# Kernel optimization log

Hardware: AMD Instinct MI355X
Metric: run time of the kernel (lower is better)

Reference implementation:

```python
import jax, jax.numpy as jnp
import numpy as np

IN_DIM = 1024
OUT_DIM = 1024
HIDDEN = 1024
T = 16384
R_MIN, R_MAX, MAX_PHASE = 0.9, 0.999, 6.28


@jax.vmap
def binary_operator_diag(q_i, q_j):
    A_i, b_i = q_i
    A_j, b_j = q_j
    return (A_j * A_i, A_j * b_i + b_j)


def setup_inputs() -> dict:
    key = jax.random.key(0)
    ks = jax.random.split(key, 8)
    inputs = jax.random.normal(ks[0], (T, IN_DIM), dtype=jnp.float32)
    # nu_log / theta_log per original initializers
    u1 = jax.random.uniform(ks[1], (HIDDEN,), dtype=jnp.float32)
    nu_log = jnp.log(-0.5 * jnp.log(u1 * (R_MAX ** 2 - R_MIN ** 2) + R_MIN ** 2))
    u2 = jax.random.uniform(ks[2], (HIDDEN,), dtype=jnp.float32)
    theta_log = jnp.log(MAX_PHASE * u2)
    diag_lambda = jnp.exp(-jnp.exp(nu_log) + 1j * jnp.exp(theta_log))
    gamma_log = jnp.log(jnp.sqrt(1 - jnp.abs(diag_lambda) ** 2))
    B_re = jax.random.normal(ks[3], (IN_DIM, HIDDEN), dtype=jnp.float32) / jnp.sqrt(2.0 * IN_DIM)
    B_im = jax.random.normal(ks[4], (IN_DIM, HIDDEN), dtype=jnp.float32) / jnp.sqrt(2.0 * IN_DIM)
    C_re = jax.random.normal(ks[5], (OUT_DIM, HIDDEN), dtype=jnp.float32) / jnp.sqrt(1.0 * HIDDEN)
    C_im = jax.random.normal(ks[6], (OUT_DIM, HIDDEN), dtype=jnp.float32) / jnp.sqrt(1.0 * HIDDEN)
    D = jax.random.normal(ks[7], (OUT_DIM, IN_DIM), dtype=jnp.float32)
    return {"inputs": inputs, "nu_log": nu_log, "theta_log": theta_log,
            "gamma_log": gamma_log, "B_re": B_re, "B_im": B_im,
            "C_re": C_re, "C_im": C_im, "D": D}


def reference(inputs, nu_log, theta_log, gamma_log, B_re, B_im, C_re, C_im, D):
    # diagonal complex transition eigenvalues, shape (H,)
    diag_lambda = jnp.exp(-jnp.exp(nu_log) + 1j * jnp.exp(theta_log))
    # NOTE: original code expands gamma on axis=-1 -> (H, 1); broadcasts against
    # B_norm (in_dim, H) because in_dim == hidden_dim. Reproduced faithfully.
    B_norm = (B_re + 1j * B_im) * jnp.exp(gamma_log)[:, None]
    C = C_re + 1j * C_im
    T_len = inputs.shape[-2]
    Lambda_elements = jnp.repeat(diag_lambda[None, :], T_len, axis=0)  # (T, H)
    Bu_elements = jnp.einsum('ih,ti->th', B_norm, inputs)              # (T, H) complex
    _, hidden_states = jax.lax.associative_scan(
        binary_operator_diag, (Lambda_elements, Bu_elements))
    outputs = jnp.real(jnp.einsum('th,oh->to', hidden_states, C))      # (T, out)
    outputs = outputs + jnp.einsum('ti,io->to', inputs, D)             # D used as 'io'
    return outputs
```

## Files before the change

kernel.cpp:

```cpp
#include <hip/hip_runtime.h>
#include <hip/hip_bf16.h>
#include <stdint.h>

#define T_LEN   16384
#define HID     1024
#define KDIM    1024
#define CHUNK   64
#define NCHUNK  256

typedef __bf16 bf16x8 __attribute__((ext_vector_type(8)));
typedef float  f32x4  __attribute__((ext_vector_type(4)));

__device__ inline ushort f2bf(float f) {
  union { float f; uint32_t u; } v; v.f = f;
  uint32_t r = v.u + 0x7FFF + ((v.u >> 16) & 1);
  return (ushort)(r >> 16);
}
__device__ inline float bf2f(ushort u) {
  union { uint32_t u; float f; } v; v.u = ((uint32_t)u) << 16;
  return v.f;
}

__device__ inline void gload16(const void* g, void* l) {
  __builtin_amdgcn_global_load_lds(
      (const __attribute__((address_space(1))) void*)g,
      (__attribute__((address_space(3))) void*)l, 16, 0, 0);
}

__global__ __launch_bounds__(256) void prep_kernel(
    const float* __restrict__ nu_log, const float* __restrict__ theta_log,
    const float* __restrict__ gamma_log,
    float* __restrict__ lam_re, float* __restrict__ lam_im, float* __restrict__ eg) {
  int h = blockIdx.x * 256 + threadIdx.x;
  if (h < HID) {
    float mag = expf(-expf(nu_log[h]));
    float th  = expf(theta_log[h]);
    lam_re[h] = mag * cosf(th);
    lam_im[h] = mag * sinf(th);
    eg[h]     = expf(gamma_log[h]);
  }
}

__global__ __launch_bounds__(256) void convX(
    const float* __restrict__ src, ushort* __restrict__ dst) {
  size_t i = ((size_t)blockIdx.x * 256 + threadIdx.x) * 4;
  float4 v = *(const float4*)(src + i);
  ushort4 o;
  o.x = f2bf(v.x); o.y = f2bf(v.y); o.z = f2bf(v.z); o.w = f2bf(v.w);
  *(ushort4*)(dst + i) = o;
}

__global__ __launch_bounds__(256) void weight_prep(
    const float* __restrict__ Bre, const float* __restrict__ Bim,
    const float* __restrict__ Cre, const float* __restrict__ Cim,
    const float* __restrict__ D,   const float* __restrict__ eg,
    ushort* __restrict__ BreT, ushort* __restrict__ BimT,
    ushort* __restrict__ CreB, ushort* __restrict__ CimB,
    ushort* __restrict__ DT) {
  __shared__ float tile[32][33];
  int z = blockIdx.z;
  if (z == 2 || z == 3) {
    const float* src = (z == 2) ? Cre : Cim;
    ushort* dst = (z == 2) ? CreB : CimB;
    float s = (z == 2) ? 1.0f : -1.0f;
    size_t base = ((size_t)blockIdx.y * 32 + (threadIdx.x >> 3)) * 1024 +
                  blockIdx.x * 32 + (threadIdx.x & 7) * 4;
    float4 v = *(const float4*)(src + base);
    ushort4 o;
    o.x = f2bf(v.x * s); o.y = f2bf(v.y * s);
    o.z = f2bf(v.z * s); o.w = f2bf(v.w * s);
    *(ushort4*)(dst + base) = o;
    return;
  }
  const float* src = (z == 0) ? Bre : (z == 1) ? Bim : D;
  ushort* dst = (z == 0) ? BreT : (z == 1) ? BimT : DT;
  bool scaled = (z < 2);
  int bx = blockIdx.x * 32;
  int by = blockIdx.y * 32;
  int tx = threadIdx.x & 31, ty = threadIdx.x >> 5;
#pragma unroll
  for (int r = 0; r < 32; r += 8)
    tile[ty + r][tx] = src[(size_t)(by + ty + r) * 1024 + bx + tx];
  __syncthreads();
  float sc = scaled ? eg[by + tx] : 1.0f;
#pragma unroll
  for (int r = 0; r < 32; r += 8)
    dst[(size_t)(bx + ty + r) * 1024 + by + tx] = f2bf(tile[tx][ty + r] * sc);
}


#define BAR()   __builtin_amdgcn_s_barrier()
#define FEN()   asm volatile("" ::: "memory")
#define VM4()   asm volatile("s_waitcnt vmcnt(4)" ::: "memory")
#define VM0()   asm volatile("s_waitcnt vmcnt(0)" ::: "memory")
#define PBAR()  do { FEN(); BAR(); FEN(); } while (0)

#define STAGE_HALF(G, LDA, R0, K0, LT, HALF)                         \
  do {                                                               \
    _Pragma("unroll")                                                \
    for (int is_ = 0; is_ < 2; ++is_) {                              \
      int seg_ = w * 2 + is_;                                        \
      int gr_ = (R0) + (HALF) * 128 + seg_ * 8 + (l >> 3);           \
      int gc_ = (K0) + (((l & 7) ^ (l >> 3)) << 3);                  \
      gload16((G) + (size_t)gr_ * (LDA) + gc_,                       \
              (LT) + (HALF) * 8192 + seg_ * 512);                    \
    }                                                                \
  } while (0)

#define DS_A(QM, BUF)                                                \
  do {                                                               \
    _Pragma("unroll")                                                \
    for (int m_ = 0; m_ < 4; ++m_) {                                 \
      int r_ = (wr * 128 + ((QM) * 4 + m_) * 16 + lo) * 64;          \
      a[m_][0] = *(const bf16x8*)((BUF) + r_ + c0us);                \
      a[m_][1] = *(const bf16x8*)((BUF) + r_ + c1us);                \
    }                                                                \
  } while (0)

#define DS_B(QN, BUF, REG)                                           \
  do {                                                               \
    _Pragma("unroll")                                                \
    for (int n_ = 0; n_ < 2; ++n_) {                                 \
      int r_ = (wc * 64 + ((QN) * 2 + n_) * 16 + lo) * 64;           \
      REG[n_][0] = *(const bf16x8*)((BUF) + r_ + c0us);              \
      REG[n_][1] = *(const bf16x8*)((BUF) + r_ + c1us);              \
    }                                                                \
  } while (0)

#define MFMA_Q(QM, QN, REG)                                          \
  do {                                                               \
    __builtin_amdgcn_s_setprio(1);                                   \
    _Pragma("unroll")                                                \
    for (int m_ = 0; m_ < 4; ++m_)                                   \
      _Pragma("unroll")                                              \
      for (int n_ = 0; n_ < 2; ++n_) {                               \
        f32x4* ac_ = &acc[(QM) * 4 + m_][(QN) * 2 + n_];             \
        *ac_ = __builtin_amdgcn_mfma_f32_16x16x32_bf16(              \
            a[m_][0], REG[n_][0], *ac_, 0, 0, 0);                    \
        *ac_ = __builtin_amdgcn_mfma_f32_16x16x32_bf16(              \
            a[m_][1], REG[n_][1], *ac_, 0, 0, 0);                    \
      }                                                              \
    __builtin_amdgcn_s_setprio(0);                                   \
  } while (0)

template<int NSEG>
__device__ __forceinline__ void gemm256_1bar(
    const ushort* Ap0, int ld0, const ushort* Bp0,
    const ushort* Ap1, int ld1, const ushort* Bp1,
    const ushort* Ap2, int ld2, const ushort* Bp2,
    ushort* lds, int row0, int col0,
    int w, int l, int wr, int wc, int lo, int c0us, int c1us,
    f32x4 (&acc)[8][4]) {
  ushort* A0 = lds;
  ushort* A1 = lds + 16384;
  ushort* B0 = lds + 32768;
  ushort* B1 = lds + 49152;
  bf16x8 a[4][2], bq0[2][2], bq1[2][2];
  const int NT = NSEG * 16;

  auto stageA = [&](int t, ushort* buf) {
    const ushort* A; int lda;
    if constexpr (NSEG == 1) { A = Ap0; lda = ld0; }
    else {
      if (t < 16)      { A = Ap0; lda = ld0; }
      else if (t < 32) { A = Ap1; lda = ld1; }
      else             { A = Ap2; lda = ld2; }
    }
    const int kk = (t & 15) * 64;
    STAGE_HALF(A, lda, row0, kk, buf, 0);
    STAGE_HALF(A, lda, row0, kk, buf, 1);
  };
  auto stageB = [&](int t, ushort* buf) {
    const ushort* B;
    if constexpr (NSEG == 1) { B = Bp0; }
    else {
      if (t < 16)      B = Bp0;
      else if (t < 32) B = Bp1;
      else             B = Bp2;
    }
    const int kk = (t & 15) * 64;
    STAGE_HALF(B, 1024, col0, kk, buf, 0);
    STAGE_HALF(B, 1024, col0, kk, buf, 1);
  };

  stageA(0, A0); stageB(0, B0); stageB(1, B1);
  VM4(); PBAR();

#pragma unroll 1
  for (int j = 0; j < NT / 2; ++j) {
    const int t1 = 2 * j + 1, t2 = 2 * j + 2, t3 = 2 * j + 3;
    const bool st = (t2 < NT);
    DS_A(0, A0); DS_B(0, B0, bq0);
    stageA(t1, A1);
    PBAR(); MFMA_Q(0, 0, bq0);
    DS_B(1, B0, bq1);
    PBAR(); MFMA_Q(0, 1, bq1);
    DS_A(1, A0);
    PBAR(); MFMA_Q(1, 0, bq0);
    if (st) { stageB(t2, B0); VM4(); } else { VM0(); }
    PBAR(); MFMA_Q(1, 1, bq1);
    DS_A(0, A1); DS_B(0, B1, bq0);
    if (st) stageA(t2, A0);
    PBAR(); MFMA_Q(0, 0, bq0);
    DS_B(1, B1, bq1);
    PBAR(); MFMA_Q(0, 1, bq1);
    DS_A(1, A1);
    PBAR(); MFMA_Q(1, 0, bq0);
    if (st) { stageB(t3, B1); VM4(); }
    PBAR(); MFMA_Q(1, 1, bq1);
  }
}

__global__ __launch_bounds__(512, 2) void gemm_bu(
    const ushort* __restrict__ A, const ushort* __restrict__ B,
    ushort* __restrict__ O) {
  __shared__ __align__(16) ushort lds[65536];
  const int tid = threadIdx.x;
  const int w = tid >> 6, l = tid & 63;
  const int wr = w >> 2, wc = w & 3;
  const int lo = l & 15, q = l >> 4;
  const int xorv = (lo & 7) << 4;
  const int c0us = ((q * 16) ^ xorv) >> 1;
  const int c1us = ((64 + q * 16) ^ xorv) >> 1;
  const int id = blockIdx.x;
  const int xcd = id & 7, slot = id >> 3;
  const int row0 = (xcd * 8 + (slot >> 3)) * 256;
  const int col0 = (slot & 7) * 256;
  f32x4 acc[8][4];
#pragma unroll
  for (int m = 0; m < 8; ++m)
#pragma unroll
    for (int n = 0; n < 4; ++n) acc[m][n] = (f32x4){0.f, 0.f, 0.f, 0.f};
  gemm256_1bar<1>(A, 1024, B, A, 1024, B, A, 1024, B,
                  lds, row0, col0, w, l, wr, wc, lo, c0us, c1us, acc);
  const int rowb = row0 + wr * 128, colb = col0 + wc * 64;
#pragma unroll
  for (int m = 0; m < 8; ++m)
#pragma unroll
    for (int n = 0; n < 4; ++n) {
      int col = colb + n * 16 + lo;
#pragma unroll
      for (int r = 0; r < 4; ++r)
        O[(size_t)(rowb + m * 16 + q * 4 + r) * 2048 + col] = f2bf(acc[m][n][r]);
    }
}

__global__ __launch_bounds__(512, 2) void gemm3(
    const ushort* __restrict__ Hall,
    const ushort* __restrict__ CreB, const ushort* __restrict__ CimB,
    const ushort* __restrict__ X,    const ushort* __restrict__ DT,
    float* __restrict__ O) {
  __shared__ __align__(16) ushort lds[65536];
  const int tid = threadIdx.x;
  const int w = tid >> 6, l = tid & 63;
  const int wr = w >> 2, wc = w & 3;
  const int lo = l & 15, q = l >> 4;
  const int xorv = (lo & 7) << 4;
  const int c0us = ((q * 16) ^ xorv) >> 1;
  const int c1us = ((64 + q * 16) ^ xorv) >> 1;
  const int id = blockIdx.x;
  const int xcd = id & 7, slot = id >> 3;
  const int row0 = (xcd * 8 + (slot >> 2)) * 256;
  const int col0 = (slot & 3) * 256;
  f32x4 acc[8][4];
#pragma unroll
  for (int m = 0; m < 8; ++m)
#pragma unroll
    for (int n = 0; n < 4; ++n) acc[m][n] = (f32x4){0.f, 0.f, 0.f, 0.f};
  gemm256_1bar<3>(Hall, 2048, CreB,
                  Hall + 1024, 2048, CimB,
                  X, 1024, DT,
                  lds, row0, col0, w, l, wr, wc, lo, c0us, c1us, acc);
  const int rowb = row0 + wr * 128, colb = col0 + wc * 64;
#pragma unroll
  for (int m = 0; m < 8; ++m)
#pragma unroll
    for (int n = 0; n < 4; ++n) {
      int col = colb + n * 16 + lo;
#pragma unroll
      for (int r = 0; r < 4; ++r)
        O[(size_t)(rowb + m * 16 + q * 4 + r) * HID + col] = acc[m][n][r];
    }
}

__global__ __launch_bounds__(256) void scan_sums(
    const ushort* __restrict__ Bu,
    const float* __restrict__ lam_re, const float* __restrict__ lam_im,
    float* __restrict__ Sre, float* __restrict__ Sim) {
  int h0 = (blockIdx.y * 256 + threadIdx.x) * 2;
  int c = blockIdx.x;
  float lr0 = lam_re[h0], li0 = lam_im[h0];
  float lr1 = lam_re[h0 + 1], li1 = lam_im[h0 + 1];
  float hr0 = 0.f, hi0 = 0.f, hr1 = 0.f, hi1 = 0.f;
  const uint* P = (const uint*)Bu;
  size_t baseR = (size_t)c * CHUNK * 1024 + (h0 >> 1);
  size_t baseI = baseR + 512;
#pragma unroll 8
  for (int t = 0; t < CHUNK; ++t) {
    uint re = P[baseR + (size_t)t * 1024];
    uint im = P[baseI + (size_t)t * 1024];
    float br0 = bf2f((ushort)re), br1 = bf2f((ushort)(re >> 16));
    float bi0 = bf2f((ushort)im), bi1 = bf2f((ushort)(im >> 16));
    float nr0 = fmaf(lr0, hr0, fmaf(-li0, hi0, br0));
    float ni0 = fmaf(lr0, hi0, fmaf(li0, hr0, bi0));
    float nr1 = fmaf(lr1, hr1, fmaf(-li1, hi1, br1));
    float ni1 = fmaf(lr1, hi1, fmaf(li1, hr1, bi1));
    hr0 = nr0; hi0 = ni0; hr1 = nr1; hi1 = ni1;
  }
  Sre[(size_t)c * HID + h0] = hr0;  Sre[(size_t)c * HID + h0 + 1] = hr1;
  Sim[(size_t)c * HID + h0] = hi0;  Sim[(size_t)c * HID + h0 + 1] = hi1;
}

__global__ __launch_bounds__(256) void scan_carry(
    const float* __restrict__ Sre, const float* __restrict__ Sim,
    const float* __restrict__ lam_re, const float* __restrict__ lam_im,
    float* __restrict__ Pre, float* __restrict__ Pim) {
  int h = blockIdx.x * 256 + threadIdx.x;
  float lr = lam_re[h], li = lam_im[h];
  float pr = lr, pi = li;
#pragma unroll
  for (int s = 0; s < 6; ++s) {
    float nr = pr * pr - pi * pi;
    float ni = 2.f * pr * pi;
    pr = nr; pi = ni;
  }
  float cr = 0.f, ci = 0.f;
  for (int c = 0; c < NCHUNK; ++c) {
    Pre[(size_t)c * HID + h] = cr;
    Pim[(size_t)c * HID + h] = ci;
    float sr = Sre[(size_t)c * HID + h];
    float si = Sim[(size_t)c * HID + h];
    float nr = fmaf(pr, cr, fmaf(-pi, ci, sr));
    float ni = fmaf(pr, ci, fmaf(pi, cr, si));
    cr = nr; ci = ni;
  }
}

__global__ __launch_bounds__(256) void scan_emit(
    const ushort* __restrict__ Bu,
    const float* __restrict__ lam_re, const float* __restrict__ lam_im,
    const float* __restrict__ Pre, const float* __restrict__ Pim,
    ushort* __restrict__ Hall) {
  int h0 = (blockIdx.y * 256 + threadIdx.x) * 2;
  int c = blockIdx.x;
  float lr0 = lam_re[h0], li0 = lam_im[h0];
  float lr1 = lam_re[h0 + 1], li1 = lam_im[h0 + 1];
  float hr0 = Pre[(size_t)c * HID + h0], hi0 = Pim[(size_t)c * HID + h0];
  float hr1 = Pre[(size_t)c * HID + h0 + 1], hi1 = Pim[(size_t)c * HID + h0 + 1];
  const uint* P = (const uint*)Bu;
  uint* Q = (uint*)Hall;
  size_t baseR = (size_t)c * CHUNK * 1024 + (h0 >> 1);
  size_t baseI = baseR + 512;
#pragma unroll 8
  for (int t = 0; t < CHUNK; ++t) {
    uint re = P[baseR + (size_t)t * 1024];
    uint im = P[baseI + (size_t)t * 1024];
    float br0 = bf2f((ushort)re), br1 = bf2f((ushort)(re >> 16));
    float bi0 = bf2f((ushort)im), bi1 = bf2f((ushort)(im >> 16));
    float nr0 = fmaf(lr0, hr0, fmaf(-li0, hi0, br0));
    float ni0 = fmaf(lr0, hi0, fmaf(li0, hr0, bi0));
    float nr1 = fmaf(lr1, hr1, fmaf(-li1, hi1, br1));
    float ni1 = fmaf(lr1, hi1, fmaf(li1, hr1, bi1));
    hr0 = nr0; hi0 = ni0; hr1 = nr1; hi1 = ni1;
    Q[baseR + (size_t)t * 1024] = (uint)f2bf(hr0) | ((uint)f2bf(hr1) << 16);
    Q[baseI + (size_t)t * 1024] = (uint)f2bf(hi0) | ((uint)f2bf(hi1) << 16);
  }
}

extern "C" void kernel_launch(void* const* d_in, const int* in_sizes, int n_in,
                              void* d_out, int out_size, void* d_ws, size_t ws_size,
                              hipStream_t stream) {
  const float* inputs    = (const float*)d_in[0];
  const float* nu_log    = (const float*)d_in[1];
  const float* theta_log = (const float*)d_in[2];
  const float* gamma_log = (const float*)d_in[3];
  const float* B_re      = (const float*)d_in[4];
  const float* B_im      = (const float*)d_in[5];
  const float* C_re      = (const float*)d_in[6];
  const float* C_im      = (const float*)d_in[7];
  const float* D         = (const float*)d_in[8];
  float* out = (float*)d_out;

  char* ws = (char*)d_ws;
  constexpr size_t TH = (size_t)T_LEN * HID;
  constexpr size_t W  = (size_t)1024 * 1024;
  constexpr size_t CH = (size_t)NCHUNK * HID;

  ushort* Xbf  = (ushort*)(ws);
  ushort* Bu   = (ushort*)(ws + TH * 2);
  ushort* Hall = (ushort*)(ws + TH * 6);
  char*   p    = ws + TH * 10;
  ushort* Ball = (ushort*)(p);             p += 2 * W * 2;
  ushort* CreB = (ushort*)(p);             p += W * 2;
  ushort* CimB = (ushort*)(p);             p += W * 2;
  ushort* DT   = (ushort*)(p);             p += W * 2;
  float*  Sre  = (float*)(p);              p += CH * 4;
  float*  Sim  = (float*)(p);              p += CH * 4;
  float*  Pre  = (float*)(p);              p += CH * 4;
  float*  Pim  = (float*)(p);              p += CH * 4;
  float*  lamR = (float*)(p);              p += 4096;
  float*  lamI = (float*)(p);              p += 4096;
  float*  eg   = (float*)(p);              p += 4096;
  ushort* BreT = Ball;
  ushort* BimT = Ball + W;

  prep_kernel<<<dim3(HID / 256), 256, 0, stream>>>(nu_log, theta_log, gamma_log,
                                                   lamR, lamI, eg);
  convX<<<dim3((unsigned)(TH / 4 / 256)), 256, 0, stream>>>(inputs, Xbf);
  weight_prep<<<dim3(32, 32, 5), 256, 0, stream>>>(B_re, B_im, C_re, C_im, D, eg,
                                                   BreT, BimT, CreB, CimB, DT);

  gemm_bu<<<dim3(512), 512, 0, stream>>>(Xbf, Ball, Bu);

  scan_sums<<<dim3(NCHUNK, HID / 512), 256, 0, stream>>>(Bu, lamR, lamI, Sre, Sim);
  scan_carry<<<dim3(HID / 256), 256, 0, stream>>>(Sre, Sim, lamR, lamI, Pre, Pim);
  scan_emit<<<dim3(NCHUNK, HID / 512), 256, 0, stream>>>(Bu, lamR, lamI, Pre, Pim,
                                                         Hall);

  gemm3<<<dim3(256), 512, 0, stream>>>(Hall, CreB, CimB, Xbf, DT, out);
}
```

Before: 340.9 us.

## Merge prep kernels and fold scan carry pass into emit kernel

Fuses the three preprocessing kernels (lambda computation, input bf16 conversion, weight transpose/scale) into one launch with a z-indexed dispatch, computing exp(gamma) inline. Removes the serial scan_carry kernel; each scan_emit block instead recomputes its chunk prefix by walking all earlier chunk sums, and scan kernels now process 4 hidden units per thread with wider loads. This trades two launches and a single-threaded serial carry pass for redundant O(c) carry work per chunk (later chunks do up to 255 steps).

Measured after the change: 378.3 us. 1.11x slower.

```diff
diff --git a/kernel.cpp b/kernel.cpp
--- a/kernel.cpp
+++ b/kernel.cpp
@@ -27,44 +27,46 @@
       (__attribute__((address_space(3))) void*)l, 16, 0, 0);
 }
 
-__global__ __launch_bounds__(256) void prep_kernel(
+__global__ __launch_bounds__(256) void prep_all(
+    const float* __restrict__ inputs,
     const float* __restrict__ nu_log, const float* __restrict__ theta_log,
     const float* __restrict__ gamma_log,
-    float* __restrict__ lam_re, float* __restrict__ lam_im, float* __restrict__ eg) {
-  int h = blockIdx.x * 256 + threadIdx.x;
-  if (h < HID) {
-    float mag = expf(-expf(nu_log[h]));
-    float th  = expf(theta_log[h]);
-    lam_re[h] = mag * cosf(th);
-    lam_im[h] = mag * sinf(th);
-    eg[h]     = expf(gamma_log[h]);
-  }
-}
-
-__global__ __launch_bounds__(256) void convX(
-    const float* __restrict__ src, ushort* __restrict__ dst) {
-  size_t i = ((size_t)blockIdx.x * 256 + threadIdx.x) * 4;
-  float4 v = *(const float4*)(src + i);
-  ushort4 o;
-  o.x = f2bf(v.x); o.y = f2bf(v.y); o.z = f2bf(v.z); o.w = f2bf(v.w);
-  *(ushort4*)(dst + i) = o;
-}
-
-__global__ __launch_bounds__(256) void weight_prep(
     const float* __restrict__ Bre, const float* __restrict__ Bim,
     const float* __restrict__ Cre, const float* __restrict__ Cim,
-    const float* __restrict__ D,   const float* __restrict__ eg,
+    const float* __restrict__ D,
+    ushort* __restrict__ Xbf,
     ushort* __restrict__ BreT, ushort* __restrict__ BimT,
     ushort* __restrict__ CreB, ushort* __restrict__ CimB,
-    ushort* __restrict__ DT) {
+    ushort* __restrict__ DT,
+    float* __restrict__ lam_re, float* __restrict__ lam_im) {
   __shared__ float tile[32][33];
-  int z = blockIdx.z;
+  const int z = blockIdx.z;
+  const int tid = threadIdx.x;
+  if (z >= 6) {
+    size_t b = (size_t)(z - 6) * 1024 + blockIdx.y * 32 + blockIdx.x;
+    size_t i = (b * 256 + tid) * 4;
+    float4 v = *(const float4*)(inputs + i);
+    ushort4 o;
+    o.x = f2bf(v.x); o.y = f2bf(v.y); o.z = f2bf(v.z); o.w = f2bf(v.w);
+    *(ushort4*)(Xbf + i) = o;
+    return;
+  }
+  if (z == 5) {
+    if (blockIdx.y == 0 && blockIdx.x < 4) {
+      int h = blockIdx.x * 256 + tid;
+      float mag = expf(-expf(nu_log[h]));
+      float th  = expf(theta_log[h]);
+      lam_re[h] = mag * cosf(th);
+      lam_im[h] = mag * sinf(th);
+    }
+    return;
+  }
   if (z == 2 || z == 3) {
     const float* src = (z == 2) ? Cre : Cim;
     ushort* dst = (z == 2) ? CreB : CimB;
     float s = (z == 2) ? 1.0f : -1.0f;
-    size_t base = ((size_t)blockIdx.y * 32 + (threadIdx.x >> 3)) * 1024 +
-                  blockIdx.x * 32 + (threadIdx.x & 7) * 4;
+    size_t base = ((size_t)blockIdx.y * 32 + (tid >> 3)) * 1024 +
+                  blockIdx.x * 32 + (tid & 7) * 4;
     float4 v = *(const float4*)(src + base);
     ushort4 o;
     o.x = f2bf(v.x * s); o.y = f2bf(v.y * s);
@@ -77,17 +79,16 @@
   bool scaled = (z < 2);
   int bx = blockIdx.x * 32;
   int by = blockIdx.y * 32;
-  int tx = threadIdx.x & 31, ty = threadIdx.x >> 5;
+  int tx = tid & 31, ty = tid >> 5;
 #pragma unroll
   for (int r = 0; r < 32; r += 8)
     tile[ty + r][tx] = src[(size_t)(by + ty + r) * 1024 + bx + tx];
   __syncthreads();
-  float sc = scaled ? eg[by + tx] : 1.0f;
+  float sc = scaled ? expf(gamma_log[by + tx]) : 1.0f;
 #pragma unroll
   for (int r = 0; r < 32; r += 8)
     dst[(size_t)(bx + ty + r) * 1024 + by + tx] = f2bf(tile[tx][ty + r] * sc);
 }
-
 
 #define BAR()   __builtin_amdgcn_s_barrier()
 #define FEN()   asm volatile("" ::: "memory")
@@ -287,83 +288,92 @@
     const ushort* __restrict__ Bu,
     const float* __restrict__ lam_re, const float* __restrict__ lam_im,
     float* __restrict__ Sre, float* __restrict__ Sim) {
-  int h0 = (blockIdx.y * 256 + threadIdx.x) * 2;
-  int c = blockIdx.x;
-  float lr0 = lam_re[h0], li0 = lam_im[h0];
-  float lr1 = lam_re[h0 + 1], li1 = lam_im[h0 + 1];
-  float hr0 = 0.f, hi0 = 0.f, hr1 = 0.f, hi1 = 0.f;
-  const uint* P = (const uint*)Bu;
-  size_t baseR = (size_t)c * CHUNK * 1024 + (h0 >> 1);
-  size_t baseI = baseR + 512;
+  const int c = blockIdx.x, tid = threadIdx.x;
+  const int h0 = tid * 4;
+  float lr[4], li[4], hr[4], hi[4];
+#pragma unroll
+  for (int j = 0; j < 4; ++j) {
+    lr[j] = lam_re[h0 + j]; li[j] = lam_im[h0 + j];
+    hr[j] = 0.f; hi[j] = 0.f;
+  }
+  const uint2* R = (const uint2*)Bu;
+  size_t rb = (size_t)c * CHUNK * 512;
 #pragma unroll 8
   for (int t = 0; t < CHUNK; ++t) {
-    uint re = P[baseR + (size_t)t * 1024];
-    uint im = P[baseI + (size_t)t * 1024];
-    float br0 = bf2f((ushort)re), br1 = bf2f((ushort)(re >> 16));
-    float bi0 = bf2f((ushort)im), bi1 = bf2f((ushort)(im >> 16));
-    float nr0 = fmaf(lr0, hr0, fmaf(-li0, hi0, br0));
-    float ni0 = fmaf(lr0, hi0, fmaf(li0, hr0, bi0));
-    float nr1 = fmaf(lr1, hr1, fmaf(-li1, hi1, br1));
-    float ni1 = fmaf(lr1, hi1, fmaf(li1, hr1, bi1));
-    hr0 = nr0; hi0 = ni0; hr1 = nr1; hi1 = ni1;
-  }
-  Sre[(size_t)c * HID + h0] = hr0;  Sre[(size_t)c * HID + h0 + 1] = hr1;
-  Sim[(size_t)c * HID + h0] = hi0;  Sim[(size_t)c * HID + h0 + 1] = hi1;
-}
-
-__global__ __launch_bounds__(256) void scan_carry(
-    const float* __restrict__ Sre, const float* __restrict__ Sim,
-    const float* __restrict__ lam_re, const float* __restrict__ lam_im,
-    float* __restrict__ Pre, float* __restrict__ Pim) {
-  int h = blockIdx.x * 256 + threadIdx.x;
-  float lr = lam_re[h], li = lam_im[h];
-  float pr = lr, pi = li;
-#pragma unroll
-  for (int s = 0; s < 6; ++s) {
-    float nr = pr * pr - pi * pi;
-    float ni = 2.f * pr * pi;
-    pr = nr; pi = ni;
-  }
-  float cr = 0.f, ci = 0.f;
-  for (int c = 0; c < NCHUNK; ++c) {
-    Pre[(size_t)c * HID + h] = cr;
-    Pim[(size_t)c * HID + h] = ci;
-    float sr = Sre[(size_t)c * HID + h];
-    float si = Sim[(size_t)c * HID + h];
-    float nr = fmaf(pr, cr, fmaf(-pi, ci, sr));
-    float ni = fmaf(pr, ci, fmaf(pi, cr, si));
-    cr = nr; ci = ni;
-  }
+    uint2 re = R[rb + (size_t)t * 512 + tid];
+    uint2 im = R[rb + (size_t)t * 512 + 256 + tid];
+    float br[4] = { bf2f((ushort)re.x), bf2f((ushort)(re.x >> 16)),
+                    bf2f((ushort)re.y), bf2f((ushort)(re.y >> 16)) };
+    float bi[4] = { bf2f((ushort)im.x), bf2f((ushort)(im.x >> 16)),
+                    bf2f((ushort)im.y), bf2f((ushort)(im.y >> 16)) };
+#pragma unroll
+    for (int j = 0; j < 4; ++j) {
+      float nr = fmaf(lr[j], hr[j], fmaf(-li[j], hi[j], br[j]));
+      float ni = fmaf(lr[j], hi[j], fmaf(li[j], hr[j], bi[j]));
+      hr[j] = nr; hi[j] = ni;
+    }
+  }
+  *(float4*)(Sre + (size_t)c * HID + h0) = (float4){hr[0], hr[1], hr[2], hr[3]};
+  *(float4*)(Sim + (size_t)c * HID + h0) = (float4){hi[0], hi[1], hi[2], hi[3]};
 }
 
 __global__ __launch_bounds__(256) void scan_emit(
     const ushort* __restrict__ Bu,
     const float* __restrict__ lam_re, const float* __restrict__ lam_im,
-    const float* __restrict__ Pre, const float* __restrict__ Pim,
+    const float* __restrict__ Sre, const float* __restrict__ Sim,
     ushort* __restrict__ Hall) {
-  int h0 = (blockIdx.y * 256 + threadIdx.x) * 2;
-  int c = blockIdx.x;
-  float lr0 = lam_re[h0], li0 = lam_im[h0];
-  float lr1 = lam_re[h0 + 1], li1 = lam_im[h0 + 1];
-  float hr0 = Pre[(size_t)c * HID + h0], hi0 = Pim[(size_t)c * HID + h0];
-  float hr1 = Pre[(size_t)c * HID + h0 + 1], hi1 = Pim[(size_t)c * HID + h0 + 1];
-  const uint* P = (const uint*)Bu;
-  uint* Q = (uint*)Hall;
-  size_t baseR = (size_t)c * CHUNK * 1024 + (h0 >> 1);
-  size_t baseI = baseR + 512;
-#pragma unroll 8
+  const int c = blockIdx.x, tid = threadIdx.x;
+  const int h0 = tid * 4;
+  float lr[4], li[4], pr[4], pi[4], hr[4], hi[4];
+#pragma unroll
+  for (int j = 0; j < 4; ++j) {
+    lr[j] = lam_re[h0 + j]; li[j] = lam_im[h0 + j];
+    float ar = lr[j], ai = li[j];
+#pragma unroll
+    for (int s = 0; s < 6; ++s) {
+      float nr = ar * ar - ai * ai;
+      float ni = 2.f * ar * ai;
+      ar = nr; ai = ni;
+    }
+    pr[j] = ar; pi[j] = ai;
+    hr[j] = 0.f; hi[j] = 0.f;
+  }
+  for (int cp = 0; cp < c; ++cp) {
+    float4 sr = *(const float4*)(Sre + (size_t)cp * HID + h0);
+    float4 si = *(const float4*)(Sim + (size_t)cp * HID + h0);
+    float srv[4] = {sr.x, sr.y, sr.z, sr.w};
+    float siv[4] = {si.x, si.y, si.z, si.w};
+#pragma unroll
+    for (int j = 0; j < 4; ++j) {
+      float nr = fmaf(pr[j], hr[j], fmaf(-pi[j], hi[j], srv[j]));
+      float ni = fmaf(pr[j], hi[j], fmaf(pi[j], hr[j], siv[j]));
+      hr[j] = nr; hi[j] = ni;
+    }
+  }
+  const uint2* R = (const uint2*)Bu;
+  uint2* Q = (uint2*)Hall;
+  size_t rb = (size_t)c * CHUNK * 512;
+#pragma unroll 4
   for (int t = 0; t < CHUNK; ++t) {
-    uint re = P[baseR + (size_t)t * 1024];
-    uint im = P[baseI + (size_t)t * 1024];
-    float br0 = bf2f((ushort)re), br1 = bf2f((ushort)(re >> 16));
-    float bi0 = bf2f((ushort)im), bi1 = bf2f((ushort)(im >> 16));
-    float nr0 = fmaf(lr0, hr0, fmaf(-li0, hi0, br0));
-    float ni0 = fmaf(lr0, hi0, fmaf(li0, hr0, bi0));
-    float nr1 = fmaf(lr1, hr1, fmaf(-li1, hi1, br1));
-    float ni1 = fmaf(lr1, hi1, fmaf(li1, hr1, bi1));
-    hr0 = nr0; hi0 = ni0; hr1 = nr1; hi1 = ni1;
-    Q[baseR + (size_t)t * 1024] = (uint)f2bf(hr0) | ((uint)f2bf(hr1) << 16);
-    Q[baseI + (size_t)t * 1024] = (uint)f2bf(hi0) | ((uint)f2bf(hi1) << 16);
+    uint2 re = R[rb + (size_t)t * 512 + tid];
+    uint2 im = R[rb + (size_t)t * 512 + 256 + tid];
+    float br[4] = { bf2f((ushort)re.x), bf2f((ushort)(re.x >> 16)),
+                    bf2f((ushort)re.y), bf2f((ushort)(re.y >> 16)) };
+    float bi[4] = { bf2f((ushort)im.x), bf2f((ushort)(im.x >> 16)),
+                    bf2f((ushort)im.y), bf2f((ushort)(im.y >> 16)) };
+#pragma unroll
+    for (int j = 0; j < 4; ++j) {
+      float nr = fmaf(lr[j], hr[j], fmaf(-li[j], hi[j], br[j]));
+      float ni = fmaf(lr[j], hi[j], fmaf(li[j], hr[j], bi[j]));
+      hr[j] = nr; hi[j] = ni;
+    }
+    uint2 oR, oI;
+    oR.x = (uint)f2bf(hr[0]) | ((uint)f2bf(hr[1]) << 16);
+    oR.y = (uint)f2bf(hr[2]) | ((uint)f2bf(hr[3]) << 16);
+    oI.x = (uint)f2bf(hi[0]) | ((uint)f2bf(hi[1]) << 16);
+    oI.y = (uint)f2bf(hi[2]) | ((uint)f2bf(hi[3]) << 16);
+    Q[rb + (size_t)t * 512 + tid] = oR;
+    Q[rb + (size_t)t * 512 + 256 + tid] = oI;
   }
 }
 
@@ -403,19 +413,16 @@
   float*  eg   = (float*)(p);              p += 4096;
   ushort* BreT = Ball;
   ushort* BimT = Ball + W;
-
-  prep_kernel<<<dim3(HID / 256), 256, 0, stream>>>(nu_log, theta_log, gamma_log,
-                                                   lamR, lamI, eg);
-  convX<<<dim3((unsigned)(TH / 4 / 256)), 256, 0, stream>>>(inputs, Xbf);
-  weight_prep<<<dim3(32, 32, 5), 256, 0, stream>>>(B_re, B_im, C_re, C_im, D, eg,
-                                                   BreT, BimT, CreB, CimB, DT);
+  (void)Pre; (void)Pim; (void)eg;
+
+  prep_all<<<dim3(32, 32, 22), 256, 0, stream>>>(
+      inputs, nu_log, theta_log, gamma_log, B_re, B_im, C_re, C_im, D,
+      Xbf, BreT, BimT, CreB, CimB, DT, lamR, lamI);
 
   gemm_bu<<<dim3(512), 512, 0, stream>>>(Xbf, Ball, Bu);
 
-  scan_sums<<<dim3(NCHUNK, HID / 512), 256, 0, stream>>>(Bu, lamR, lamI, Sre, Sim);
-  scan_carry<<<dim3(HID / 256), 256, 0, stream>>>(Sre, Sim, lamR, lamI, Pre, Pim);
-  scan_emit<<<dim3(NCHUNK, HID / 512), 256, 0, stream>>>(Bu, lamR, lamI, Pre, Pim,
-                                                         Hall);
+  scan_sums<<<dim3(NCHUNK), 256, 0, stream>>>(Bu, lamR, lamI, Sre, Sim);
+  scan_emit<<<dim3(NCHUNK), 256, 0, stream>>>(Bu, lamR, lamI, Sre, Sim, Hall);
 
   gemm3<<<dim3(256), 512, 0, stream>>>(Hall, CreB, CimB, Xbf, DT, out);
 }
```
